# Kernel tuning notes

Hardware: AMD Instinct MI355X
Metric: run time of the kernel (lower is better)

## Reference

```python
import jax, jax.numpy as jnp
import numpy as np

N_NODES = 100000


def _sage_conv(x, src, dst, Wl, bl, Wr):
    # PyG SAGEConv (aggr='mean', root_weight=True):
    # out_i = Wl @ mean_{j in N(i)} x_j + bl + Wr @ x_i
    msg = x[src]                                              # [E, F] gather
    s = jax.ops.segment_sum(msg, dst, num_segments=N_NODES)   # [N, F] scatter-add
    cnt = jax.ops.segment_sum(jnp.ones((src.shape[0], 1), x.dtype), dst,
                              num_segments=N_NODES)           # [N, 1]
    mean = s / jnp.maximum(cnt, 1.0)                          # empty nbhd -> 0
    return mean @ Wl + bl + x @ Wr


def setup_inputs() -> dict:
    key = jax.random.key(0)
    ks = jax.random.split(key, 8)
    N, E, F = N_NODES, 1600000, 128
    x = jax.random.normal(ks[0], (N, F), dtype=jnp.float32)
    edge_index = jax.random.randint(ks[1], (2, E), 0, N, dtype=jnp.int64)
    def lin(k, fi, fo):
        return jax.random.normal(k, (fi, fo), dtype=jnp.float32) / np.sqrt(fi)
    return {
        "x": x, "edge_index": edge_index,
        "Wl0": lin(ks[2], F, F), "bl0": jnp.zeros((F,), jnp.float32), "Wr0": lin(ks[3], F, F),
        "Wl1": lin(ks[4], F, F), "bl1": jnp.zeros((F,), jnp.float32), "Wr1": lin(ks[5], F, F),
        "Wl2": lin(ks[6], F, F), "bl2": jnp.zeros((F,), jnp.float32), "Wr2": lin(ks[7], F, F),
    }


def reference(x, edge_index, Wl0, bl0, Wr0, Wl1, bl1, Wr1, Wl2, bl2, Wr2):
    src, dst = edge_index[0], edge_index[1]
    # layers 0..num_layers-2: SAGEConv -> ReLU -> dropout(eval=identity)
    h = jax.nn.relu(_sage_conv(x, src, dst, Wl0, bl0, Wr0))
    h = jax.nn.relu(_sage_conv(h, src, dst, Wl1, bl1, Wr1))
    # final layer: no activation
    out = _sage_conv(h, src, dst, Wl2, bl2, Wr2)
    return out
```

## Files before the change

### kernel.cpp

```cpp
#include <hip/hip_runtime.h>
#include <stdint.h>

#define NN 100000
#define FF 128
#define NB 391

typedef __bf16 bf16x8 __attribute__((ext_vector_type(8)));
typedef float f32x4 __attribute__((ext_vector_type(4)));

__device__ __forceinline__ unsigned short f2bf(float f) {
    unsigned int u = __float_as_uint(f);
    u += 0x7FFF + ((u >> 16) & 1);
    return (unsigned short)(u >> 16);
}
__device__ __forceinline__ float bf2f(unsigned short b) {
    return __uint_as_float(((unsigned int)b) << 16);
}

__device__ __forceinline__ int edge_at(const void* ei, int idx, int is64) {
    if (is64) return (int)((const long long*)ei)[idx];
    return ((const int*)ei)[idx];
}

__global__ void init_kernel(const unsigned int* ei, int* flag, int* bcnt) {
    __shared__ int any;
    int t = threadIdx.x;
    if (t == 0) any = 0;
    for (int i = t; i < NB; i += 512) bcnt[i] = 0;
    __syncthreads();
    unsigned int v = ei[2 * t + 1];
    if (v != 0u) atomicOr(&any, 1);
    __syncthreads();
    if (t == 0) *flag = (any ? 0 : 1);
}

__global__ void bcount_prep_kernel(const void* ei, const int* flag, int* bcnt, int E,
                                   const float* __restrict__ x, unsigned short* __restrict__ xb,
                                   const float* Wl0, const float* Wr0,
                                   const float* Wl1, const float* Wr1,
                                   const float* Wl2, const float* Wr2,
                                   unsigned short* __restrict__ whi) {
    if (blockIdx.x < 256) {
        __shared__ int h[NB];
        for (int i = threadIdx.x; i < NB; i += 256) h[i] = 0;
        __syncthreads();
        int is64 = *flag;
        int stride = 256 * 256;
        for (int e = blockIdx.x * 256 + threadIdx.x; e < E; e += stride)
            atomicAdd(&h[edge_at(ei, E + e, is64) >> 8], 1);
        __syncthreads();
        for (int i = threadIdx.x; i < NB; i += 256) {
            int v = h[i];
            if (v) atomicAdd(&bcnt[i], v);
        }
    } else {
        int gid = (blockIdx.x - 256) * 256 + threadIdx.x;
        int gstride = (gridDim.x - 256) * 256;
        const int PC = NN * FF / 8;
        for (int i = gid; i < PC; i += gstride) {
            float4 a = ((const float4*)x)[i * 2];
            float4 b = ((const float4*)x)[i * 2 + 1];
            ushort4 p0 = make_ushort4(f2bf(a.x), f2bf(a.y), f2bf(a.z), f2bf(a.w));
            ushort4 p1 = make_ushort4(f2bf(b.x), f2bf(b.y), f2bf(b.z), f2bf(b.w));
            ((ushort4*)xb)[i * 2] = p0;
            ((ushort4*)xb)[i * 2 + 1] = p1;
        }
        const int WT = 3 * 256 * FF;
        for (int i = gid; i < WT; i += gstride) {
            int l = i >> 15;
            int rem = i & 32767;
            int n = rem >> 7;
            int k = rem & 127;
            const float* Wl = l == 0 ? Wl0 : (l == 1 ? Wl1 : Wl2);
            const float* Wr = l == 0 ? Wr0 : (l == 1 ? Wr1 : Wr2);
            float v = (n < FF) ? Wl[k * FF + n] : Wr[k * FF + (n - FF)];
            whi[i] = f2bf(v);
        }
    }
}

__global__ void bscan_kernel(const int* bcnt, int* bbase, int* bcursor,
                             int* rowptr, int E) {
    __shared__ int s[512];
    int t = threadIdx.x;
    int v = (t < NB) ? bcnt[t] : 0;
    s[t] = v;
    __syncthreads();
    for (int off = 1; off < 512; off <<= 1) {
        int u = (t >= off) ? s[t - off] : 0;
        __syncthreads();
        s[t] += u;
        __syncthreads();
    }
    if (t <= NB) {
        int excl = (t == 0) ? 0 : s[t - 1];
        bbase[t] = excl;
        if (t < NB) bcursor[t] = excl;
    }
    if (t == 0) rowptr[NN] = E;
}

__global__ void bscatter_kernel(const void* ei, const int* flag, int* bcursor,
                                unsigned int* packed, int E, int CH) {
    __shared__ int cnt[NB];
    __shared__ int base[NB];
    int t = threadIdx.x;
    for (int i = t; i < NB; i += 256) cnt[i] = 0;
    __syncthreads();
    int is64 = *flag;
    int beg = blockIdx.x * CH;
    int end = min(E, beg + CH);
    for (int e = beg + t; e < end; e += 256)
        atomicAdd(&cnt[edge_at(ei, E + e, is64) >> 8], 1);
    __syncthreads();
    for (int i = t; i < NB; i += 256) {
        int c = cnt[i];
        base[i] = c ? atomicAdd(&bcursor[i], c) : 0;
    }
    __syncthreads();
    for (int i = t; i < NB; i += 256) cnt[i] = 0;
    __syncthreads();
    for (int e = beg + t; e < end; e += 256) {
        int sV = edge_at(ei, e, is64);
        int d  = edge_at(ei, E + e, is64);
        int b = d >> 8;
        int pos = base[b] + atomicAdd(&cnt[b], 1);
        packed[pos] = ((unsigned int)sV << 8) | (unsigned int)(d & 255);
    }
}

__global__ void bfill_kernel(const unsigned int* __restrict__ packed,
                             const int* __restrict__ bbase,
                             int* __restrict__ rowptr, int* __restrict__ col) {
    __shared__ int cnt[256];
    __shared__ int scn[256];
    __shared__ int exc[256];
    int t = threadIdx.x;
    int b = blockIdx.x;
    int ebeg = bbase[b], eend = bbase[b + 1];
    cnt[t] = 0;
    __syncthreads();
    for (int e = ebeg + t; e < eend; e += 256)
        atomicAdd(&cnt[packed[e] & 255], 1);
    __syncthreads();
    int v = cnt[t];
    scn[t] = v;
    __syncthreads();
    for (int off = 1; off < 256; off <<= 1) {
        int u = (t >= off) ? scn[t - off] : 0;
        __syncthreads();
        scn[t] += u;
        __syncthreads();
    }
    int excl = scn[t] - v;
    exc[t] = excl;
    int node = b * 256 + t;
    if (node < NN) rowptr[node] = ebeg + excl;
    cnt[t] = 0;
    __syncthreads();
    for (int e = ebeg + t; e < eend; e += 256) {
        unsigned int p = packed[e];
        int l = p & 255;
        int pos = ebeg + exc[l] + atomicAdd(&cnt[l], 1);
        col[pos] = (int)(p >> 8);
    }
}

__device__ __forceinline__ unsigned int rowld(const unsigned short* __restrict__ h,
                                              int c, int lbyte) {
    return *(const unsigned int*)((const char*)h + ((size_t)(unsigned)c << 8) + lbyte);
}

__global__ void aggregate_kernel(const unsigned short* __restrict__ h,
                                 const int* __restrict__ rowptr,
                                 const int* __restrict__ col,
                                 unsigned short* __restrict__ m) {
    int gw = (int)((blockIdx.x * blockDim.x + threadIdx.x) >> 6);
    gw = __builtin_amdgcn_readfirstlane(gw);
    if (gw >= NN) return;
    const int lane = (int)(threadIdx.x & 63);
    const int lbyte = lane * 4;
    int beg = __builtin_amdgcn_readfirstlane(rowptr[gw]);
    int end = __builtin_amdgcn_readfirstlane(rowptr[gw + 1]);
    int deg = end - beg;
    float a0 = 0.f, a1 = 0.f;

    int done = 0;
    while (done < deg) {
        int batch = min(deg - done, 64);
        int colv = 0;
        if (lane < batch) colv = __builtin_nontemporal_load(&col[beg + done + lane]);

        auto LD = [&](int i) -> unsigned int {
            return rowld(h, __builtin_amdgcn_readlane(colv, i), lbyte);
        };

        unsigned int u0 = 0, u1 = 0, u2 = 0, u3 = 0;
        unsigned int u4 = 0, u5 = 0, u6 = 0, u7 = 0;
        u0 = LD(0);
        if (batch > 1) u1 = LD(1);
        if (batch > 2) u2 = LD(2);
        if (batch > 3) u3 = LD(3);
        if (batch > 4) u4 = LD(4);
        if (batch > 5) u5 = LD(5);
        if (batch > 6) u6 = LD(6);
        if (batch > 7) u7 = LD(7);
        for (int i = 0; i < batch; i += 4) {
            unsigned int n0 = 0, n1 = 0, n2 = 0, n3 = 0;
            if (i + 8  < batch) n0 = LD(i + 8);
            if (i + 9  < batch) n1 = LD(i + 9);
            if (i + 10 < batch) n2 = LD(i + 10);
            if (i + 11 < batch) n3 = LD(i + 11);
            a0 += __uint_as_float(u0 << 16);
            a1 += __uint_as_float(u0 & 0xffff0000u);
            a0 += __uint_as_float(u1 << 16);
            a1 += __uint_as_float(u1 & 0xffff0000u);
            a0 += __uint_as_float(u2 << 16);
            a1 += __uint_as_float(u2 & 0xffff0000u);
            a0 += __uint_as_float(u3 << 16);
            a1 += __uint_as_float(u3 & 0xffff0000u);
            u0 = u4; u1 = u5; u2 = u6; u3 = u7;
            u4 = n0; u5 = n1; u6 = n2; u7 = n3;
        }
        done += batch;
    }

    float r = deg > 0 ? 1.f / (float)deg : 0.f;
    unsigned int p = (unsigned int)f2bf(a0 * r) | ((unsigned int)f2bf(a1 * r) << 16);
    __builtin_nontemporal_store(p,
        (unsigned int*)((char*)m + ((size_t)gw << 8) + lbyte));
}

template <int WMODE>
__global__ __launch_bounds__(256, 6) void gemm_mfma_kernel(
        const unsigned short* __restrict__ mb,
        const unsigned short* __restrict__ hb,
        const unsigned short* __restrict__ w2,
        const float* __restrict__ bl,
        void* __restrict__ outp) {
    __shared__ __align__(16) char smem[16384];

    const int t = threadIdx.x;
    const int lane = t & 63;
    const int wid = t >> 6;
    const int m0 = blockIdx.x * 64;
    const int n0w = wid * 32;

    f32x4 acc[4][2];
    #pragma unroll
    for (int mr = 0; mr < 4; ++mr)
        #pragma unroll
        for (int nr = 0; nr < 2; ++nr) acc[mr][nr] = (f32x4){0.f, 0.f, 0.f, 0.f};

    const int srow = t >> 2;
    const int sk8 = (t & 3) * 8;
    const int arow = lane & 15;
    const int kg = (lane >> 4) * 8;

    uint4 pfM, pfH;
    auto issueA = [&](int kc) {
        int gr = m0 + srow; if (gr >= NN) gr = NN - 1;
        size_t ga = (size_t)gr * FF + kc * 32 + sk8;
        pfM = *(const uint4*)(mb + ga);
        pfH = *(const uint4*)(hb + ga);
    };

    issueA(0);
    for (int kc = 0; kc < 4; ++kc) {
        __syncthreads();
        *(uint4*)(smem +        srow * 80 + sk8 * 2) = pfM;
        *(uint4*)(smem + 5120 + srow * 80 + sk8 * 2) = pfH;
        if (kc < 3) issueA(kc + 1);
        __syncthreads();

        bf16x8 wfrag[4];
        #pragma unroll
        for (int nr = 0; nr < 2; ++nr) {
            int n = n0w + nr * 16 + arow;
            wfrag[nr * 2 + 0] = *(const bf16x8*)(w2 + (size_t)n * FF + kc * 32 + kg);
            wfrag[nr * 2 + 1] = *(const bf16x8*)(w2 + (size_t)(128 + n) * FF + kc * 32 + kg);
        }
        const int kg2 = (lane >> 4) * 16;
        #pragma unroll
        for (int mr = 0; mr < 4; ++mr) {
            int row = mr * 16 + arow;
            bf16x8 a_m = *(const bf16x8*)(smem +        row * 80 + kg2);
            bf16x8 a_h = *(const bf16x8*)(smem + 5120 + row * 80 + kg2);
            #pragma unroll
            for (int nr = 0; nr < 2; ++nr) {
                acc[mr][nr] = __builtin_amdgcn_mfma_f32_16x16x32_bf16(wfrag[nr * 2 + 0], a_m, acc[mr][nr], 0, 0, 0);
                acc[mr][nr] = __builtin_amdgcn_mfma_f32_16x16x32_bf16(wfrag[nr * 2 + 1], a_h, acc[mr][nr], 0, 0, 0);
            }
        }
    }

    const int nodeL = lane & 15;
    const int rg4 = (lane >> 4) * 4;
    if (WMODE == 0) {
        __syncthreads();
        #pragma unroll
        for (int nr = 0; nr < 2; ++nr) {
            int n = n0w + nr * 16 + rg4;
            float4 bias = *(const float4*)(bl + n);
            int g = n >> 2;
            #pragma unroll
            for (int mr = 0; mr < 4; ++mr) {
                int row = mr * 16 + nodeL;
                f32x4 a = acc[mr][nr];
                float o0 = fmaxf(a[0] + bias.x, 0.f), o1 = fmaxf(a[1] + bias.y, 0.f);
                float o2 = fmaxf(a[2] + bias.z, 0.f), o3 = fmaxf(a[3] + bias.w, 0.f);
                ushort4 p = make_ushort4(f2bf(o0), f2bf(o1), f2bf(o2), f2bf(o3));
                *(ushort4*)(smem + row * 256 + ((g ^ ((row & 7) << 2)) << 3)) = p;
            }
        }
        __syncthreads();
        unsigned short* hout = (unsigned short*)outp;
        #pragma unroll
        for (int it = 0; it < 8; ++it) {
            int idx = t + it * 256;
            int row = idx >> 5;
            int g = idx & 31;
            int node = m0 + row;
            if (node < NN) {
                ushort4 v = *(const ushort4*)(smem + row * 256 + ((g ^ ((row & 7) << 2)) << 3));
                *(ushort4*)(hout + (size_t)node * FF + g * 4) = v;
            }
        }
    } else {
        float* fout = (float*)outp;
        #pragma unroll
        for (int r = 0; r < 2; ++r) {
            __syncthreads();
            #pragma unroll
            for (int nr = 0; nr < 2; ++nr) {
                int n = n0w + nr * 16 + rg4;
                float4 bias = *(const float4*)(bl + n);
                int g = n >> 2;
                #pragma unroll
                for (int mr = 2 * r; mr < 2 * r + 2; ++mr) {
                    int lrow = mr * 16 + nodeL - 32 * r;
                    f32x4 a = acc[mr][nr];
                    float4 p = make_float4(a[0] + bias.x, a[1] + bias.y,
                                           a[2] + bias.z, a[3] + bias.w);
                    *(float4*)(smem + lrow * 512 + ((g ^ (lrow & 7)) << 4)) = p;
                }
            }
            __syncthreads();
            #pragma unroll
            for (int it = 0; it < 4; ++it) {
                int idx = t + it * 256;
                int lrow = idx >> 5;
                int g = idx & 31;
                int node = m0 + 32 * r + lrow;
                if (node < NN) {
                    float4 v = *(const float4*)(smem + lrow * 512 + ((g ^ (lrow & 7)) << 4));
                    *(float4*)(fout + (size_t)node * FF + g * 4) = v;
                }
            }
        }
    }
}

extern "C" void kernel_launch(void* const* d_in, const int* in_sizes, int n_in,
                              void* d_out, int out_size, void* d_ws, size_t ws_size,
                              hipStream_t stream) {
    const float* x   = (const float*)d_in[0];
    const void*  ei  = d_in[1];
    const float* Wl0 = (const float*)d_in[2];
    const float* bl0 = (const float*)d_in[3];
    const float* Wr0 = (const float*)d_in[4];
    const float* Wl1 = (const float*)d_in[5];
    const float* bl1 = (const float*)d_in[6];
    const float* Wr1 = (const float*)d_in[7];
    const float* Wl2 = (const float*)d_in[8];
    const float* bl2 = (const float*)d_in[9];
    const float* Wr2 = (const float*)d_in[10];
    float* out = (float*)d_out;
    const int E = in_sizes[1] / 2;

    char* w = (char*)d_ws;
    size_t off = 0;
    auto alloc = [&](size_t bytes) {
        void* p = w + off;
        off += (bytes + 511) & ~(size_t)511;
        return p;
    };
    int*            flag    = (int*)alloc(4);
    int*            bcnt    = (int*)alloc(sizeof(int) * NB);
    int*            bbase   = (int*)alloc(sizeof(int) * (NB + 1));
    int*            bcursor = (int*)alloc(sizeof(int) * NB);
    int*            rowptr  = (int*)alloc(sizeof(int) * (NN + 1));
    unsigned int*   packed  = (unsigned int*)alloc(sizeof(int) * E);
    int*            col     = (int*)alloc(sizeof(int) * E);
    unsigned short* whi     = (unsigned short*)alloc(sizeof(short) * 3 * 256 * FF);
    unsigned short* xb      = (unsigned short*)alloc(sizeof(short) * (size_t)NN * FF);
    unsigned short* mbuf    = (unsigned short*)alloc(sizeof(short) * (size_t)NN * FF);
    unsigned short* hA      = (unsigned short*)alloc(sizeof(short) * (size_t)NN * FF);
    unsigned short* hB      = xb;

    init_kernel<<<1, 512, 0, stream>>>((const unsigned int*)ei, flag, bcnt);
    bcount_prep_kernel<<<1280, 256, 0, stream>>>(ei, flag, bcnt, E,
                                                 x, xb, Wl0, Wr0, Wl1, Wr1, Wl2, Wr2, whi);
    bscan_kernel<<<1, 512, 0, stream>>>(bcnt, bbase, bcursor, rowptr, E);
    int CH = (E + 255) / 256;
    bscatter_kernel<<<256, 256, 0, stream>>>(ei, flag, bcursor, packed, E, CH);
    bfill_kernel<<<NB, 256, 0, stream>>>(packed, bbase, rowptr, col);

    int gb = (NN + 63) / 64;
    int ab = (NN * 64 + 255) / 256;

    aggregate_kernel<<<ab, 256, 0, stream>>>(xb, rowptr, col, mbuf);
    gemm_mfma_kernel<0><<<gb, 256, 0, stream>>>(mbuf, xb, whi + 0 * 256 * FF, bl0, hA);
    aggregate_kernel<<<ab, 256, 0, stream>>>(hA, rowptr, col, mbuf);
    gemm_mfma_kernel<0><<<gb, 256, 0, stream>>>(mbuf, hA, whi + 1 * 256 * FF, bl1, hB);
    aggregate_kernel<<<ab, 256, 0, stream>>>(hB, rowptr, col, mbuf);
    gemm_mfma_kernel<1><<<gb, 256, 0, stream>>>(mbuf, hB, whi + 2 * 256 * FF, bl2, out);
}
```

Before: 320.8 us.

## Fuse neighbor mean aggregation into the MFMA GEMM kernel per layer

Combines the per-node mean aggregation and the dual-weight MFMA GEMM into one kernel per layer. Each block aggregates its 64 destination rows into a swizzled LDS tile and loads its own root rows, then runs the GEMM from LDS. This removes the intermediate mean buffer's global write and read plus three kernel launches. In exchange, each wave now aggregates 16 nodes serially, so fewer independent waves are in flight to hide gather latency. Higher LDS use (32KB) and launch bounds lowered from 6 to 4 also reduce occupancy for the latency-bound gather.

```diff
diff --git a/kernel.cpp b/kernel.cpp
--- a/kernel.cpp
+++ b/kernel.cpp
@@ -171,108 +171,97 @@
     return *(const unsigned int*)((const char*)h + ((size_t)(unsigned)c << 8) + lbyte);
 }
 
-__global__ void aggregate_kernel(const unsigned short* __restrict__ h,
-                                 const int* __restrict__ rowptr,
-                                 const int* __restrict__ col,
-                                 unsigned short* __restrict__ m) {
-    int gw = (int)((blockIdx.x * blockDim.x + threadIdx.x) >> 6);
-    gw = __builtin_amdgcn_readfirstlane(gw);
-    if (gw >= NN) return;
-    const int lane = (int)(threadIdx.x & 63);
-    const int lbyte = lane * 4;
-    int beg = __builtin_amdgcn_readfirstlane(rowptr[gw]);
-    int end = __builtin_amdgcn_readfirstlane(rowptr[gw + 1]);
-    int deg = end - beg;
-    float a0 = 0.f, a1 = 0.f;
-
-    int done = 0;
-    while (done < deg) {
-        int batch = min(deg - done, 64);
-        int colv = 0;
-        if (lane < batch) colv = __builtin_nontemporal_load(&col[beg + done + lane]);
-
-        auto LD = [&](int i) -> unsigned int {
-            return rowld(h, __builtin_amdgcn_readlane(colv, i), lbyte);
-        };
-
-        unsigned int u0 = 0, u1 = 0, u2 = 0, u3 = 0;
-        unsigned int u4 = 0, u5 = 0, u6 = 0, u7 = 0;
-        u0 = LD(0);
-        if (batch > 1) u1 = LD(1);
-        if (batch > 2) u2 = LD(2);
-        if (batch > 3) u3 = LD(3);
-        if (batch > 4) u4 = LD(4);
-        if (batch > 5) u5 = LD(5);
-        if (batch > 6) u6 = LD(6);
-        if (batch > 7) u7 = LD(7);
-        for (int i = 0; i < batch; i += 4) {
-            unsigned int n0 = 0, n1 = 0, n2 = 0, n3 = 0;
-            if (i + 8  < batch) n0 = LD(i + 8);
-            if (i + 9  < batch) n1 = LD(i + 9);
-            if (i + 10 < batch) n2 = LD(i + 10);
-            if (i + 11 < batch) n3 = LD(i + 11);
-            a0 += __uint_as_float(u0 << 16);
-            a1 += __uint_as_float(u0 & 0xffff0000u);
-            a0 += __uint_as_float(u1 << 16);
-            a1 += __uint_as_float(u1 & 0xffff0000u);
-            a0 += __uint_as_float(u2 << 16);
-            a1 += __uint_as_float(u2 & 0xffff0000u);
-            a0 += __uint_as_float(u3 << 16);
-            a1 += __uint_as_float(u3 & 0xffff0000u);
-            u0 = u4; u1 = u5; u2 = u6; u3 = u7;
-            u4 = n0; u5 = n1; u6 = n2; u7 = n3;
-        }
-        done += batch;
-    }
-
-    float r = deg > 0 ? 1.f / (float)deg : 0.f;
-    unsigned int p = (unsigned int)f2bf(a0 * r) | ((unsigned int)f2bf(a1 * r) << 16);
-    __builtin_nontemporal_store(p,
-        (unsigned int*)((char*)m + ((size_t)gw << 8) + lbyte));
-}
-
 template <int WMODE>
-__global__ __launch_bounds__(256, 6) void gemm_mfma_kernel(
-        const unsigned short* __restrict__ mb,
+__global__ __launch_bounds__(256, 4) void fused_layer_kernel(
         const unsigned short* __restrict__ hb,
         const unsigned short* __restrict__ w2,
         const float* __restrict__ bl,
+        const int* __restrict__ rowptr,
+        const int* __restrict__ col,
         void* __restrict__ outp) {
-    __shared__ __align__(16) char smem[16384];
+    __shared__ __align__(16) char smem[32768];
 
     const int t = threadIdx.x;
     const int lane = t & 63;
     const int wid = t >> 6;
     const int m0 = blockIdx.x * 64;
+
+    #pragma unroll
+    for (int i = 0; i < 4; ++i) {
+        int row = i * 16 + (t >> 4);
+        int ch = (t & 15) * 16;
+        int gr = m0 + row; if (gr >= NN) gr = NN - 1;
+        uint4 v = *(const uint4*)((const char*)hb + (size_t)gr * 256 + ch);
+        *(uint4*)(smem + 16384 + row * 256 + (ch ^ ((row & 7) << 4))) = v;
+    }
+
+    const int lbyte = lane * 4;
+    for (int s = 0; s < 16; ++s) {
+        int row = wid * 16 + s;
+        int gw = m0 + row;
+        float a0 = 0.f, a1 = 0.f;
+        int deg = 0;
+        if (gw < NN) {
+            int beg = __builtin_amdgcn_readfirstlane(rowptr[gw]);
+            int end = __builtin_amdgcn_readfirstlane(rowptr[gw + 1]);
+            deg = end - beg;
+            int done = 0;
+            while (done < deg) {
+                int batch = min(deg - done, 64);
+                int colv = 0;
+                if (lane < batch) colv = __builtin_nontemporal_load(&col[beg + done + lane]);
+                auto LD = [&](int i) -> unsigned int {
+                    return rowld(hb, __builtin_amdgcn_readlane(colv, i), lbyte);
+                };
+                unsigned int u0 = 0, u1 = 0, u2 = 0, u3 = 0;
+                unsigned int u4 = 0, u5 = 0, u6 = 0, u7 = 0;
+                u0 = LD(0);
+                if (batch > 1) u1 = LD(1);
+                if (batch > 2) u2 = LD(2);
+                if (batch > 3) u3 = LD(3);
+                if (batch > 4) u4 = LD(4);
+                if (batch > 5) u5 = LD(5);
+                if (batch > 6) u6 = LD(6);
+                if (batch > 7) u7 = LD(7);
+                for (int i = 0; i < batch; i += 4) {
+                    unsigned int n0 = 0, n1 = 0, n2 = 0, n3 = 0;
+                    if (i + 8  < batch) n0 = LD(i + 8);
+                    if (i + 9  < batch) n1 = LD(i + 9);
+                    if (i + 10 < batch) n2 = LD(i + 10);
+                    if (i + 11 < batch) n3 = LD(i + 11);
+                    a0 += __uint_as_float(u0 << 16);
+                    a1 += __uint_as_float(u0 & 0xffff0000u);
+                    a0 += __uint_as_float(u1 << 16);
+                    a1 += __uint_as_float(u1 & 0xffff0000u);
+                    a0 += __uint_as_float(u2 << 16);
+                    a1 += __uint_as_float(u2 & 0xffff0000u);
+                    a0 += __uint_as_float(u3 << 16);
+                    a1 += __uint_as_float(u3 & 0xffff0000u);
+                    u0 = u4; u1 = u5; u2 = u6; u3 = u7;
+                    u4 = n0; u5 = n1; u6 = n2; u7 = n3;
+                }
+                done += batch;
+            }
+        }
+        float r = deg > 0 ? 1.f / (float)deg : 0.f;
+        unsigned int p = (unsigned int)f2bf(a0 * r) | ((unsigned int)f2bf(a1 * r) << 16);
+        *(unsigned int*)(smem + row * 256 + (lbyte ^ ((row & 7) << 4))) = p;
+    }
+    __syncthreads();
+
     const int n0w = wid * 32;
-
     f32x4 acc[4][2];
     #pragma unroll
     for (int mr = 0; mr < 4; ++mr)
         #pragma unroll
         for (int nr = 0; nr < 2; ++nr) acc[mr][nr] = (f32x4){0.f, 0.f, 0.f, 0.f};
 
-    const int srow = t >> 2;
-    const int sk8 = (t & 3) * 8;
     const int arow = lane & 15;
     const int kg = (lane >> 4) * 8;
-
-    uint4 pfM, pfH;
-    auto issueA = [&](int kc) {
-        int gr = m0 + srow; if (gr >= NN) gr = NN - 1;
-        size_t ga = (size_t)gr * FF + kc * 32 + sk8;
-        pfM = *(const uint4*)(mb + ga);
-        pfH = *(const uint4*)(hb + ga);
-    };
-
-    issueA(0);
+    const int kg2 = (lane >> 4) * 16;
+
+    #pragma unroll
     for (int kc = 0; kc < 4; ++kc) {
-        __syncthreads();
-        *(uint4*)(smem +        srow * 80 + sk8 * 2) = pfM;
-        *(uint4*)(smem + 5120 + srow * 80 + sk8 * 2) = pfH;
-        if (kc < 3) issueA(kc + 1);
-        __syncthreads();
-
         bf16x8 wfrag[4];
         #pragma unroll
         for (int nr = 0; nr < 2; ++nr) {
@@ -280,12 +269,13 @@
             wfrag[nr * 2 + 0] = *(const bf16x8*)(w2 + (size_t)n * FF + kc * 32 + kg);
             wfrag[nr * 2 + 1] = *(const bf16x8*)(w2 + (size_t)(128 + n) * FF + kc * 32 + kg);
         }
-        const int kg2 = (lane >> 4) * 16;
         #pragma unroll
         for (int mr = 0; mr < 4; ++mr) {
             int row = mr * 16 + arow;
-            bf16x8 a_m = *(const bf16x8*)(smem +        row * 80 + kg2);
-            bf16x8 a_h = *(const bf16x8*)(smem + 5120 + row * 80 + kg2);
+            int b = kc * 64 + kg2;
+            int sb = b ^ ((row & 7) << 4);
+            bf16x8 a_m = *(const bf16x8*)(smem +         row * 256 + sb);
+            bf16x8 a_h = *(const bf16x8*)(smem + 16384 + row * 256 + sb);
             #pragma unroll
             for (int nr = 0; nr < 2; ++nr) {
                 acc[mr][nr] = __builtin_amdgcn_mfma_f32_16x16x32_bf16(wfrag[nr * 2 + 0], a_m, acc[mr][nr], 0, 0, 0);
@@ -394,7 +384,6 @@
     int*            col     = (int*)alloc(sizeof(int) * E);
     unsigned short* whi     = (unsigned short*)alloc(sizeof(short) * 3 * 256 * FF);
     unsigned short* xb      = (unsigned short*)alloc(sizeof(short) * (size_t)NN * FF);
-    unsigned short* mbuf    = (unsigned short*)alloc(sizeof(short) * (size_t)NN * FF);
     unsigned short* hA      = (unsigned short*)alloc(sizeof(short) * (size_t)NN * FF);
     unsigned short* hB      = xb;
 
@@ -407,12 +396,8 @@
     bfill_kernel<<<NB, 256, 0, stream>>>(packed, bbase, rowptr, col);
 
     int gb = (NN + 63) / 64;
-    int ab = (NN * 64 + 255) / 256;
-
-    aggregate_kernel<<<ab, 256, 0, stream>>>(xb, rowptr, col, mbuf);
-    gemm_mfma_kernel<0><<<gb, 256, 0, stream>>>(mbuf, xb, whi + 0 * 256 * FF, bl0, hA);
-    aggregate_kernel<<<ab, 256, 0, stream>>>(hA, rowptr, col, mbuf);
-    gemm_mfma_kernel<0><<<gb, 256, 0, stream>>>(mbuf, hA, whi + 1 * 256 * FF, bl1, hB);
-    aggregate_kernel<<<ab, 256, 0, stream>>>(hB, rowptr, col, mbuf);
-    gemm_mfma_kernel<1><<<gb, 256, 0, stream>>>(mbuf, hB, whi + 2 * 256 * FF, bl2, out);
-}
+
+    fused_layer_kernel<0><<<gb, 256, 0, stream>>>(xb, whi + 0 * 256 * FF, bl0, rowptr, col, hA);
+    fused_layer_kernel<0><<<gb, 256, 0, stream>>>(hA, whi + 1 * 256 * FF, bl1, rowptr, col, hB);
+    fused_layer_kernel<1><<<gb, 256, 0, stream>>>(hB, whi + 2 * 256 * FF, bl2, rowptr, col, out);
+}
```

New measurement: 391.8 us. 22.1% more time.
